# Optimization experiments

Hardware: AMD Instinct MI355X
Metric: run time of the kernel (lower is better)

Reference implementation:

```python
import jax, jax.numpy as jnp
import numpy as np

# ---- constants matching init_kwargs ----
ATOM_DIMS = np.array([119, 5, 12, 12, 10, 6, 6, 2, 2])
OFFSETS = np.concatenate([[0], np.cumsum(ATOM_DIMS)[:-1]])  # per-column offsets into concat table
HID = 256
HEADS = 8
BASES = 4
AGGS = 3  # sum, mean, max
LAYERS = 4
FH = HID // HEADS  # 32
N_GRAPHS = 2048
EPS = 1e-5


def setup_inputs() -> dict:
    key = jax.random.key(0)
    ks = iter(jax.random.split(key, 64))
    N, E = 50000, 800000
    x = jax.random.randint(next(ks), (N, 9), 0, 2, dtype=jnp.int64) if jax.config.jax_enable_x64 else jax.random.randint(next(ks), (N, 9), 0, 2, dtype=jnp.int32)
    edge_index = jax.random.randint(next(ks), (2, E), 0, N, dtype=x.dtype)
    batch = jnp.sort(jax.random.randint(next(ks), (N,), 0, N_GRAPHS, dtype=x.dtype))
    s = 0.05
    atom_emb = jax.random.normal(next(ks), (int(ATOM_DIMS.sum()), HID), jnp.float32) * s
    bases_W = jax.random.normal(next(ks), (LAYERS, HID, BASES * FH), jnp.float32) * s
    comb_W = jax.random.normal(next(ks), (LAYERS, HID, HEADS * BASES * AGGS), jnp.float32) * s
    comb_b = jnp.zeros((LAYERS, HEADS * BASES * AGGS), jnp.float32)
    conv_bias = jnp.zeros((LAYERS, HID), jnp.float32)
    bn_gamma = jnp.ones((LAYERS, HID), jnp.float32)
    bn_beta = jnp.zeros((LAYERS, HID), jnp.float32)
    w1 = jax.random.normal(next(ks), (HID, HID // 2), jnp.float32) * s
    g1 = jnp.ones((HID // 2,), jnp.float32)
    b1 = jnp.zeros((HID // 2,), jnp.float32)
    w2 = jax.random.normal(next(ks), (HID // 2, HID // 4), jnp.float32) * s
    g2 = jnp.ones((HID // 4,), jnp.float32)
    b2 = jnp.zeros((HID // 4,), jnp.float32)
    w3 = jax.random.normal(next(ks), (HID // 4, 1), jnp.float32) * s
    b3 = jnp.zeros((1,), jnp.float32)
    return dict(atom_emb=atom_emb, bases_W=bases_W, comb_W=comb_W, comb_b=comb_b,
                conv_bias=conv_bias, bn_gamma=bn_gamma, bn_beta=bn_beta,
                w1=w1, g1=g1, b1=b1, w2=w2, g2=g2, b2=b2, w3=w3, b3=b3,
                x=x, edge_index=edge_index, batch=batch)


def _bn(h, gamma, beta):
    mu = h.mean(0)
    var = h.var(0)
    return (h - mu) * jax.lax.rsqrt(var + EPS) * gamma + beta


def reference(atom_emb, bases_W, comb_W, comb_b, conv_bias, bn_gamma, bn_beta,
              w1, g1, b1, w2, g2, b2, w3, b3, x, edge_index, batch):
    N = x.shape[0]
    offs = jnp.asarray(OFFSETS, dtype=x.dtype)
    # AtomEncoder: sum of per-column embeddings (concat table + offsets)
    h = atom_emb[x + offs[None, :]].sum(axis=1)  # [N, HID]

    # edges with self-loops (EGConv add_self_loops=True); adj_t transposed: row=dst
    loop = jnp.arange(N, dtype=edge_index.dtype)
    dst = jnp.concatenate([edge_index[0], loop])
    src = jnp.concatenate([edge_index[1], loop])
    deg = jax.ops.segment_sum(jnp.ones_like(dst, jnp.float32), dst, num_segments=N)  # >=1

    for l in range(LAYERS):
        bases = h @ bases_W[l]                      # [N, B*FH]
        wts = (h @ comb_W[l] + comb_b[l]).reshape(N, HEADS, AGGS * BASES)
        msgs = bases[src]                            # [E+N, B*FH]
        agg_sum = jax.ops.segment_sum(msgs, dst, num_segments=N)
        agg_mean = agg_sum / deg[:, None]
        agg_max = jax.ops.segment_max(msgs, dst, num_segments=N)
        agg = jnp.stack([agg_sum, agg_mean, agg_max], axis=1)  # [N, A, B*FH]
        agg = agg.reshape(N, AGGS * BASES, FH)
        out = jnp.einsum('nhk,nkd->nhd', wts, agg).reshape(N, HID) + conv_bias[l]
        out = jax.nn.relu(_bn(out, bn_gamma[l], bn_beta[l]))
        h = h + out

    # global mean pool
    gsum = jax.ops.segment_sum(h, batch, num_segments=N_GRAPHS)
    gcnt = jax.ops.segment_sum(jnp.ones((N,), jnp.float32), batch, num_segments=N_GRAPHS)
    g = gsum / jnp.maximum(gcnt, 1.0)[:, None]

    z = jax.nn.relu(_bn(g @ w1, g1, b1))
    z = jax.nn.relu(_bn(z @ w2, g2, b2))
    return z @ w3 + b3
```

## Files before the change

### kernel.cpp

```cpp
#include <hip/hip_runtime.h>
#include <hip/hip_bf16.h>

#define HID 256
#define NGRAPH 2048

typedef __attribute__((ext_vector_type(8))) short s16x8;
typedef __attribute__((ext_vector_type(4))) float f32x4v;

__device__ inline short f2b(float f) {
    __hip_bfloat16 b = __float2bfloat16(f);
    return *reinterpret_cast<short*>(&b);
}
__device__ inline float b2f_lo(unsigned int v) {
    return __uint_as_float(v << 16);
}
__device__ inline float b2f_hi(unsigned int v) {
    return __uint_as_float(v & 0xffff0000u);
}

__global__ __launch_bounds__(256) void atom_enc(const int* __restrict__ x,
                                                const float* __restrict__ emb,
                                                float* __restrict__ h,
                                                short* __restrict__ hb, int N) {
    int n = blockIdx.x;
    int c = threadIdx.x;
    if (n >= N) return;
    const int offs[9] = {0, 119, 124, 136, 148, 158, 164, 170, 172};
    float s = 0.f;
#pragma unroll
    for (int j = 0; j < 9; ++j) {
        int row = x[n * 9 + j] + offs[j];
        s += emb[row * 256 + c];
    }
    h[n * 256 + c] = s;
    hb[n * 256 + c] = f2b(s);
}

__global__ void prep_wt(const float* __restrict__ bases_W, const float* __restrict__ comb_W,
                        short* __restrict__ WT) {
    int l = blockIdx.x / 224;
    int n = blockIdx.x % 224;
    int k = threadIdx.x;
    float v = (n < 128) ? bases_W[((size_t)l * 256 + k) * 128 + n]
                        : comb_W[((size_t)l * 256 + k) * 96 + (n - 128)];
    WT[((size_t)l * 224 + n) * 256 + k] = f2b(v);
}

__global__ void init_cnt(int* cnt, int N) {
    int i = blockIdx.x * blockDim.x + threadIdx.x;
    if (i < N) cnt[i] = 1;
}

__global__ void csr_count(const int* __restrict__ ei, int E, int* cnt) {
    int e = blockIdx.x * blockDim.x + threadIdx.x;
    if (e >= E) return;
    atomicAdd(&cnt[ei[e]], 1);
}

__global__ __launch_bounds__(256) void scan_s1(const int* __restrict__ cnt, int* __restrict__ blksum, int N) {
    __shared__ int red[256];
    int base = blockIdx.x * 1024;
    int s = 0;
#pragma unroll
    for (int q = 0; q < 4; ++q) {
        int i = base + threadIdx.x * 4 + q;
        s += (i < N) ? cnt[i] : 0;
    }
    red[threadIdx.x] = s;
    __syncthreads();
    for (int off = 128; off > 0; off >>= 1) {
        if (threadIdx.x < off) red[threadIdx.x] += red[threadIdx.x + off];
        __syncthreads();
    }
    if (threadIdx.x == 0) blksum[blockIdx.x] = red[0];
}

__global__ __launch_bounds__(256) void scan_s2(int* __restrict__ blksum, int nb, int* __restrict__ row_ptr, int N) {
    __shared__ int buf[256];
    int v = (threadIdx.x < nb) ? blksum[threadIdx.x] : 0;
    buf[threadIdx.x] = v;
    __syncthreads();
    for (int off = 1; off < 256; off <<= 1) {
        int t = (threadIdx.x >= off) ? buf[threadIdx.x - off] : 0;
        __syncthreads();
        buf[threadIdx.x] += t;
        __syncthreads();
    }
    if (threadIdx.x < nb) blksum[threadIdx.x] = buf[threadIdx.x] - v;
    if (threadIdx.x == 0) row_ptr[N] = buf[255];
}

__global__ __launch_bounds__(256) void scan_s3(const int* __restrict__ cnt, const int* __restrict__ blksum,
                                               int* __restrict__ row_ptr, int* __restrict__ woff, int N) {
    __shared__ int buf[256];
    int base = blockIdx.x * 1024;
    int i0 = base + threadIdx.x * 4;
    int v[4];
    int s = 0;
#pragma unroll
    for (int q = 0; q < 4; ++q) {
        int i = i0 + q;
        v[q] = (i < N) ? cnt[i] : 0;
        s += v[q];
    }
    buf[threadIdx.x] = s;
    __syncthreads();
    for (int off = 1; off < 256; off <<= 1) {
        int t = (threadIdx.x >= off) ? buf[threadIdx.x - off] : 0;
        __syncthreads();
        buf[threadIdx.x] += t;
        __syncthreads();
    }
    int excl = buf[threadIdx.x] - s + blksum[blockIdx.x];
#pragma unroll
    for (int q = 0; q < 4; ++q) {
        int i = i0 + q;
        if (i < N) { row_ptr[i] = excl; woff[i] = excl; }
        excl += v[q];
    }
}

__global__ __launch_bounds__(256) void ph_hist(const int* __restrict__ ei, int E, int T,
                                               int PB, int NBK, int* __restrict__ mcnt) {
    __shared__ int hist[256];
    hist[threadIdx.x] = 0;
    __syncthreads();
    int base = blockIdx.x * 4096;
#pragma unroll
    for (int q = 0; q < 16; ++q) {
        int i = base + q * 256 + threadIdx.x;
        if (i < T) {
            int d = (i < E) ? ei[i] : (i - E);
            atomicAdd(&hist[d >> 8], 1);
        }
    }
    __syncthreads();
    if (threadIdx.x < NBK) mcnt[threadIdx.x * PB + blockIdx.x] = hist[threadIdx.x];
}

__global__ __launch_bounds__(256) void ph_scatter(const int* __restrict__ ei, int E, int T,
                                                  int PB, int NBK, const int* __restrict__ moff,
                                                  uint2* __restrict__ pairs) {
    __shared__ int off[256];
    if (threadIdx.x < NBK) off[threadIdx.x] = moff[threadIdx.x * PB + blockIdx.x];
    __syncthreads();
    int base = blockIdx.x * 4096;
#pragma unroll
    for (int q = 0; q < 16; ++q) {
        int i = base + q * 256 + threadIdx.x;
        if (i < T) {
            int d, s;
            if (i < E) { d = ei[i]; s = ei[E + i]; }
            else       { d = i - E; s = i - E; }
            int pos = atomicAdd(&off[d >> 8], 1);
            pairs[pos] = make_uint2((unsigned)d, (unsigned)s);
        }
    }
}

__global__ __launch_bounds__(256) void ph_sort(const uint2* __restrict__ pairs,
                                               const int* __restrict__ row_ptr,
                                               const int* __restrict__ moff,
                                               int NBK, int PB, int T,
                                               int* __restrict__ srcs) {
    __shared__ int wcnt[256];
    wcnt[threadIdx.x] = 0;
    __syncthreads();
    int bin = blockIdx.x;
    int p0 = moff[bin * PB];
    int p1 = (bin + 1 < NBK) ? moff[(bin + 1) * PB] : T;
    for (int i = p0 + threadIdx.x; i < p1; i += 256) {
        uint2 u = pairs[i];
        int d = (int)u.x;
        int rank = atomicAdd(&wcnt[d & 255], 1);
        srcs[row_ptr[d] + rank] = (int)u.y;
    }
}

__global__ __launch_bounds__(256) void gemm_mfma(const short* __restrict__ hb,
                                                 const short* __restrict__ WT,
                                                 const float* __restrict__ cb,
                                                 short* __restrict__ bases,
                                                 float* __restrict__ wts, int N) {
    __shared__ short bs[2][32 * 256];
    int tid = threadIdx.x;
    int wid = tid >> 6;
    int lane = tid & 63;
    int m0 = blockIdx.x * 64 + wid * 16;
    int row_a = m0 + (lane & 15);
    if (row_a > N - 1) row_a = N - 1;
    int kgrp = (lane >> 4) * 8;

    s16x8 a[8];
#pragma unroll
    for (int i = 0; i < 8; ++i)
        a[i] = *(const s16x8*)&hb[(size_t)row_a * 256 + i * 32 + kgrp];

    int st_col = tid >> 3;
    int st_kk = (tid & 7) * 32;
    int st_sw = (st_col & 7) << 4;
    int st_base = st_col * 512 + st_kk * 2;

    auto stage = [&](int buf, int t) {
        const s16x8* src = (const s16x8*)&WT[(size_t)(t * 32 + st_col) * 256 + st_kk];
        char* dst = (char*)bs[buf];
#pragma unroll
        for (int q = 0; q < 4; ++q)
            *(s16x8*)(dst + ((st_base + q * 16) ^ st_sw)) = src[q];
    };

    stage(0, 0);

    int col = lane & 15;
    int rd_base = col * 512 + (lane >> 4) * 16;
    int rd_sw = (col & 7) << 4;
    int rbase = m0 + (lane >> 4) * 4;

    for (int t = 0; t < 7; ++t) {
        __syncthreads();
        if (t + 1 < 7) stage((t + 1) & 1, t + 1);

        const char* base = (const char*)bs[t & 1];
        f32x4v c0 = {0.f, 0.f, 0.f, 0.f};
        f32x4v c1 = {0.f, 0.f, 0.f, 0.f};
#pragma unroll
        for (int i = 0; i < 8; ++i) {
            s16x8 b0 = *(const s16x8*)(base + ((rd_base + i * 64) ^ rd_sw));
            s16x8 b1 = *(const s16x8*)(base + ((rd_base + 8192 + i * 64) ^ rd_sw));
            c0 = __builtin_amdgcn_mfma_f32_16x16x32_bf16(a[i], b0, c0, 0, 0, 0);
            c1 = __builtin_amdgcn_mfma_f32_16x16x32_bf16(a[i], b1, c1, 0, 0, 0);
        }

        int cc0 = t * 32 + col;
        int cc1 = cc0 + 16;
        float cb0 = (cc0 >= 128) ? cb[cc0 - 128] : 0.f;
        float cb1 = (cc1 >= 128) ? cb[cc1 - 128] : 0.f;
#pragma unroll
        for (int r = 0; r < 4; ++r) {
            int row = rbase + r;
            if (row >= N) continue;
            float v0 = c0[r], v1 = c1[r];
            if (cc0 < 128) bases[(size_t)row * 128 + cc0] = f2b(v0);
            else wts[(size_t)row * 96 + (cc0 - 128)] = v0 + cb0;
            if (cc1 < 128) bases[(size_t)row * 128 + cc1] = f2b(v1);
            else wts[(size_t)row * 96 + (cc1 - 128)] = v1 + cb1;
        }
    }
}

__global__ __launch_bounds__(256) void agg_einsum(const short* __restrict__ bases,
                                                  const float* __restrict__ wts,
                                                  const int* __restrict__ row_ptr,
                                                  const int* __restrict__ srcs,
                                                  const float* __restrict__ cbias,
                                                  float* __restrict__ outp,
                                                  float* __restrict__ partial, int N) {
    __shared__ float agg_lds[4][3][128];
    __shared__ float wts_lds[4][96];
    __shared__ float red[4][256];
    int wid = threadIdx.x >> 6;
    int lane = threadIdx.x & 63;
    int n = blockIdx.x * 4 + wid;
    bool valid = (n < N);

    int r0 = 0, r1 = 0;
    if (valid) {
        r0 = row_ptr[n];
        r1 = row_ptr[n + 1];
        wts_lds[wid][lane] = wts[(size_t)n * 96 + lane];
        if (lane < 32) wts_lds[wid][64 + lane] = wts[(size_t)n * 96 + 64 + lane];
    }

    int g = lane & 31;
    int half = lane >> 5;
    const short* bp = bases + 4 * g;
    const float NI = -3.402823466e+38f;
    float sA0 = 0.f, sA1 = 0.f, sA2 = 0.f, sA3 = 0.f;
    float sB0 = 0.f, sB1 = 0.f, sB2 = 0.f, sB3 = 0.f;
    float mA0 = NI, mA1 = NI, mA2 = NI, mA3 = NI;
    float mB0 = NI, mB1 = NI, mB2 = NI, mB3 = NI;

#define GACC8(S, s0_, s1_, s2_, s3_, m0_, m1_, m2_, m3_)                     \
    {                                                                        \
        uint2 v = *(const uint2*)&bp[(size_t)(S) * 128];                     \
        float f0 = b2f_lo(v.x), f1 = b2f_hi(v.x);                            \
        float f2 = b2f_lo(v.y), f3 = b2f_hi(v.y);                            \
        s0_ += f0; s1_ += f1; s2_ += f2; s3_ += f3;                          \
        m0_ = fmaxf(m0_, f0); m1_ = fmaxf(m1_, f1);                          \
        m2_ = fmaxf(m2_, f2); m3_ = fmaxf(m3_, f3);                          \
    }

    int r = r0;
    while (r < r1) {
        int chunk = r1 - r;
        if (chunk > 64) chunk = 64;
        int sidx = (lane < chunk) ? srcs[r + lane] : 0;
        int npair = chunk >> 1;
        int jp = 0;
        for (; jp + 4 <= npair; jp += 4) {
            int e0 = (jp + 0) * 2 + half, e1 = (jp + 1) * 2 + half;
            int e2 = (jp + 2) * 2 + half, e3 = (jp + 3) * 2 + half;
            int s0 = __shfl(sidx, e0), s1 = __shfl(sidx, e1);
            int s2 = __shfl(sidx, e2), s3 = __shfl(sidx, e3);
            GACC8(s0, sA0, sA1, sA2, sA3, mA0, mA1, mA2, mA3);
            GACC8(s1, sB0, sB1, sB2, sB3, mB0, mB1, mB2, mB3);
            GACC8(s2, sA0, sA1, sA2, sA3, mA0, mA1, mA2, mA3);
            GACC8(s3, sB0, sB1, sB2, sB3, mB0, mB1, mB2, mB3);
        }
        for (; jp < npair; ++jp) {
            int e0 = jp * 2 + half;
            int s0 = __shfl(sidx, e0);
            GACC8(s0, sA0, sA1, sA2, sA3, mA0, mA1, mA2, mA3);
        }
        if (chunk & 1) {
            int s0 = __shfl(sidx, chunk - 1);
            if (half == 0) {
                GACC8(s0, sB0, sB1, sB2, sB3, mB0, mB1, mB2, mB3);
            }
        }
        r += chunk;
    }
#undef GACC8

    float accs[4] = {0.f, 0.f, 0.f, 0.f};
    if (valid) {
        float s0 = sA0 + sB0, s1 = sA1 + sB1, s2 = sA2 + sB2, s3 = sA3 + sB3;
        float m0 = fmaxf(mA0, mB0), m1 = fmaxf(mA1, mB1);
        float m2 = fmaxf(mA2, mB2), m3 = fmaxf(mA3, mB3);
        s0 += __shfl_xor(s0, 32); s1 += __shfl_xor(s1, 32);
        s2 += __shfl_xor(s2, 32); s3 += __shfl_xor(s3, 32);
        m0 = fmaxf(m0, __shfl_xor(m0, 32)); m1 = fmaxf(m1, __shfl_xor(m1, 32));
        m2 = fmaxf(m2, __shfl_xor(m2, 32)); m3 = fmaxf(m3, __shfl_xor(m3, 32));

        float inv = 1.0f / (float)(r1 - r0);
        if (half == 0) {
            float4 sv = make_float4(s0, s1, s2, s3);
            float4 mv = make_float4(s0 * inv, s1 * inv, s2 * inv, s3 * inv);
            float4 xv = make_float4(m0, m1, m2, m3);
            *(float4*)&agg_lds[wid][0][4 * g] = sv;
            *(float4*)&agg_lds[wid][1][4 * g] = mv;
            *(float4*)&agg_lds[wid][2][4 * g] = xv;
        }

        asm volatile("s_waitcnt lgkmcnt(0)" ::: "memory");

#pragma unroll
        for (int j = 0; j < 4; ++j) {
            int o = lane + 64 * j;
            int hh = o >> 5;
            int d = o & 31;
            float acc = cbias[o];
#pragma unroll
            for (int k = 0; k < 12; ++k)
                acc = fmaf(wts_lds[wid][hh * 12 + k], agg_lds[wid][k >> 2][(k & 3) * 32 + d], acc);
            outp[n * 256 + o] = acc;
            accs[j] = acc;
        }
    }
#pragma unroll
    for (int j = 0; j < 4; ++j) red[wid][lane + 64 * j] = accs[j];
    __syncthreads();
    int c = threadIdx.x;
    float s = (red[0][c] + red[1][c]) + (red[2][c] + red[3][c]);
    float s2 = (red[0][c] * red[0][c] + red[1][c] * red[1][c]) +
               (red[2][c] * red[2][c] + red[3][c] * red[3][c]);
    partial[((size_t)blockIdx.x * 2 + 0) * 256 + c] = s;
    partial[((size_t)blockIdx.x * 2 + 1) * 256 + c] = s2;
}

__global__ __launch_bounds__(256) void bn_reduce(const float* __restrict__ partial, int NB,
                                                 float* __restrict__ partial2) {
    int t = threadIdx.x;
    int chunk = (NB + 255) / 256;
    int rbeg = blockIdx.x * chunk;
    int rend = min(NB, rbeg + chunk);
    float s = 0.f, s2 = 0.f;
    for (int r = rbeg; r < rend; ++r) {
        s += partial[((size_t)r * 2 + 0) * 256 + t];
        s2 += partial[((size_t)r * 2 + 1) * 256 + t];
    }
    partial2[((size_t)blockIdx.x * 2 + 0) * 256 + t] = s;
    partial2[((size_t)blockIdx.x * 2 + 1) * 256 + t] = s2;
}

__global__ void bn_stats(const float* __restrict__ v, int N, int C, float* __restrict__ partial) {
    int c = threadIdx.x;
    float s = 0.f, s2 = 0.f;
    for (int r = blockIdx.x; r < N; r += gridDim.x) {
        float t = v[r * C + c];
        s += t; s2 += t * t;
    }
    partial[(blockIdx.x * 2 + 0) * C + c] = s;
    partial[(blockIdx.x * 2 + 1) * C + c] = s2;
}

__global__ __launch_bounds__(256) void bn_finalize(const float* __restrict__ partial, int NB, int C, int N,
                                                   const float* __restrict__ gamma, const float* __restrict__ beta,
                                                   float* __restrict__ ss) {
    int c = blockIdx.x;
    float s = 0.f, s2 = 0.f;
    for (int b = threadIdx.x; b < NB; b += 256) {
        s += partial[((size_t)b * 2 + 0) * C + c];
        s2 += partial[((size_t)b * 2 + 1) * C + c];
    }
#pragma unroll
    for (int off = 32; off > 0; off >>= 1) {
        s += __shfl_down(s, off);
        s2 += __shfl_down(s2, off);
    }
    __shared__ float wsum[4][2];
    int wid = threadIdx.x >> 6;
    int lane = threadIdx.x & 63;
    if (lane == 0) { wsum[wid][0] = s; wsum[wid][1] = s2; }
    __syncthreads();
    if (threadIdx.x == 0) {
        s = (wsum[0][0] + wsum[1][0]) + (wsum[2][0] + wsum[3][0]);
        s2 = (wsum[0][1] + wsum[1][1]) + (wsum[2][1] + wsum[3][1]);
        float invN = 1.0f / (float)N;
        float mu = s * invN;
        float var = fmaxf(s2 * invN - mu * mu, 0.f);
        float sc = gamma[c] * rsqrtf(var + 1e-5f);
        ss[c] = sc;
        ss[C + c] = beta[c] - mu * sc;
    }
}

__global__ void bn_apply_res4(float4* __restrict__ h, const float4* __restrict__ outp,
                              const float* __restrict__ ss, short* __restrict__ hb,
                              int total4, int write_hb) {
    int i = blockIdx.x * blockDim.x + threadIdx.x;
    if (i >= total4) return;
    int c0 = (i * 4) & 255;
    float4 o = outp[i];
    float4 hv = h[i];
    hv.x += fmaxf(o.x * ss[c0 + 0] + ss[256 + c0 + 0], 0.f);
    hv.y += fmaxf(o.y * ss[c0 + 1] + ss[256 + c0 + 1], 0.f);
    hv.z += fmaxf(o.z * ss[c0 + 2] + ss[256 + c0 + 2], 0.f);
    hv.w += fmaxf(o.w * ss[c0 + 3] + ss[256 + c0 + 3], 0.f);
    h[i] = hv;
    if (write_hb) {
        short4 hb4;
        hb4.x = f2b(hv.x); hb4.y = f2b(hv.y); hb4.z = f2b(hv.z); hb4.w = f2b(hv.w);
        *(short4*)&hb[(size_t)i * 4] = hb4;
    }
}

__global__ void bn_apply(float* __restrict__ z, const float* __restrict__ ss, int total, int C, int Cmask) {
    int i = blockIdx.x * blockDim.x + threadIdx.x;
    if (i >= total) return;
    int c = i & Cmask;
    z[i] = fmaxf(z[i] * ss[c] + ss[C + c], 0.f);
}

__device__ int lower_bound_dev(const int* a, int n, int v) {
    int lo = 0, hi = n;
    while (lo < hi) {
        int mid = (lo + hi) >> 1;
        if (a[mid] < v) lo = mid + 1; else hi = mid;
    }
    return lo;
}

__global__ __launch_bounds__(256) void pool_kernel(const float* __restrict__ h,
                                                   const int* __restrict__ batch, int N,
                                                   float* __restrict__ g) {
    __shared__ int sh[2];
    if (threadIdx.x == 0) {
        sh[0] = lower_bound_dev(batch, N, (int)blockIdx.x);
        sh[1] = lower_bound_dev(batch, N, (int)blockIdx.x + 1);
    }
    __syncthreads();
    int s0 = sh[0], s1 = sh[1];
    float s = 0.f;
    for (int r = s0; r < s1; ++r) s += h[r * 256 + threadIdx.x];
    float cnt = (float)(s1 - s0);
    g[blockIdx.x * 256 + threadIdx.x] = s / fmaxf(cnt, 1.0f);
}

__global__ void mlp_gemm(const float* __restrict__ in, const float* __restrict__ W,
                         float* __restrict__ outp, int K, int C) {
    extern __shared__ float srow[];
    int r = blockIdx.x;
    for (int k = threadIdx.x; k < K; k += blockDim.x) srow[k] = in[r * K + k];
    __syncthreads();
    int c = threadIdx.x;
    float acc = 0.f;
    for (int k = 0; k < K; ++k) acc = fmaf(srow[k], W[k * C + c], acc);
    outp[r * C + c] = acc;
}

__global__ void final_gemm(const float* __restrict__ z2, const float* __restrict__ w3,
                           const float* __restrict__ b3, float* __restrict__ outp, int G) {
    int g = blockIdx.x * blockDim.x + threadIdx.x;
    if (g >= G) return;
    float acc = b3[0];
    for (int k = 0; k < 64; ++k) acc = fmaf(z2[g * 64 + k], w3[k], acc);
    outp[g] = acc;
}

extern "C" void kernel_launch(void* const* d_in, const int* in_sizes, int n_in,
                              void* d_out, int out_size, void* d_ws, size_t ws_size,
                              hipStream_t stream) {
    const float* atom_emb = (const float*)d_in[0];
    const float* bases_W = (const float*)d_in[1];
    const float* comb_W = (const float*)d_in[2];
    const float* comb_b = (const float*)d_in[3];
    const float* conv_bias = (const float*)d_in[4];
    const float* bn_gamma = (const float*)d_in[5];
    const float* bn_beta = (const float*)d_in[6];
    const float* w1 = (const float*)d_in[7];
    const float* g1 = (const float*)d_in[8];
    const float* b1 = (const float*)d_in[9];
    const float* w2 = (const float*)d_in[10];
    const float* g2 = (const float*)d_in[11];
    const float* b2 = (const float*)d_in[12];
    const float* w3 = (const float*)d_in[13];
    const float* b3 = (const float*)d_in[14];
    const int* x = (const int*)d_in[15];
    const int* edge_index = (const int*)d_in[16];
    const int* batch = (const int*)d_in[17];
    float* out = (float*)d_out;

    const int N = in_sizes[15] / 9;
    const int E = in_sizes[16] / 2;
    const int G = NGRAPH;
    const int T = E + N;
    const int NCHUNK = (N + 1023) / 1024;
    const int PB = (T + 4095) / 4096;
    const int NBK = (N + 255) >> 8;
    const int M = NBK * PB;
    const int MCHUNK = (M + 1023) / 1024;
    const int AGG_NB = (N + 3) / 4;

    char* p = (char*)d_ws;
    auto alloc = [&](size_t bytes) -> void* {
        void* r = (void*)p;
        p += (bytes + 255) & ~(size_t)255;
        return r;
    };
    float* h = (float*)alloc((size_t)N * 256 * 4);
    short* hb = (short*)alloc((size_t)N * 256 * 2);
    float* outb = (float*)alloc((size_t)N * 256 * 4);
    short* bases = (short*)alloc((size_t)N * 128 * 2);
    float* wts = (float*)alloc((size_t)N * 96 * 4);
    short* WT = (short*)alloc((size_t)4 * 224 * 256 * 2);
    int* row_ptr = (int*)alloc((size_t)(N + 1) * 4);
    int* cnt = (int*)alloc((size_t)N * 4);
    int* woff = (int*)alloc((size_t)N * 4);
    int* blksum = (int*)alloc((size_t)256 * 4);
    int* mcnt = (int*)alloc((size_t)(M + 1) * 4);
    int* moff = (int*)alloc((size_t)(M + 1) * 4);
    int* srcs = (int*)alloc((size_t)T * 4);
    float* partial = (float*)alloc((size_t)AGG_NB * 2 * 256 * 4);
    float* partial2 = (float*)alloc((size_t)256 * 2 * 256 * 4);
    float* ss = (float*)alloc((size_t)2 * 256 * 4);
    float* g = (float*)alloc((size_t)G * 256 * 4);
    float* z1 = (float*)alloc((size_t)G * 128 * 4);
    float* z2 = (float*)alloc((size_t)G * 64 * 4);
    uint2* pairs = (uint2*)outb;

    atom_enc<<<N, 256, 0, stream>>>(x, atom_emb, h, hb, N);
    prep_wt<<<4 * 224, 256, 0, stream>>>(bases_W, comb_W, WT);

    init_cnt<<<(N + 255) / 256, 256, 0, stream>>>(cnt, N);
    csr_count<<<(E + 255) / 256, 256, 0, stream>>>(edge_index, E, cnt);
    scan_s1<<<NCHUNK, 256, 0, stream>>>(cnt, blksum, N);
    scan_s2<<<1, 256, 0, stream>>>(blksum, NCHUNK, row_ptr, N);
    scan_s3<<<NCHUNK, 256, 0, stream>>>(cnt, blksum, row_ptr, woff, N);

    ph_hist<<<PB, 256, 0, stream>>>(edge_index, E, T, PB, NBK, mcnt);
    scan_s1<<<MCHUNK, 256, 0, stream>>>(mcnt, blksum, M);
    scan_s2<<<1, 256, 0, stream>>>(blksum, MCHUNK, moff, M);
    scan_s3<<<MCHUNK, 256, 0, stream>>>(mcnt, blksum, moff, moff, M);
    ph_scatter<<<PB, 256, 0, stream>>>(edge_index, E, T, PB, NBK, moff, pairs);
    ph_sort<<<NBK, 256, 0, stream>>>(pairs, row_ptr, moff, NBK, PB, T, srcs);

    for (int l = 0; l < 4; ++l) {
        const short* WTl = WT + (size_t)l * 224 * 256;
        const float* cb = comb_b + (size_t)l * 96;
        const float* cbias = conv_bias + (size_t)l * 256;
        const float* gam = bn_gamma + (size_t)l * 256;
        const float* bet = bn_beta + (size_t)l * 256;

        gemm_mfma<<<(N + 63) / 64, 256, 0, stream>>>(hb, WTl, cb, bases, wts, N);
        agg_einsum<<<AGG_NB, 256, 0, stream>>>(bases, wts, row_ptr, srcs, cbias, outb, partial, N);
        bn_reduce<<<256, 256, 0, stream>>>(partial, AGG_NB, partial2);
        bn_finalize<<<256, 256, 0, stream>>>(partial2, 256, 256, N, gam, bet, ss);
        int total4 = N * 256 / 4;
        bn_apply_res4<<<(total4 + 255) / 256, 256, 0, stream>>>((float4*)h, (const float4*)outb, ss, hb,
                                                                total4, l < 3 ? 1 : 0);
    }

    pool_kernel<<<G, 256, 0, stream>>>(h, batch, N, g);

    mlp_gemm<<<G, 128, 256 * 4, stream>>>(g, w1, z1, 256, 128);
    bn_stats<<<64, 128, 0, stream>>>(z1, G, 128, partial);
    bn_finalize<<<128, 256, 0, stream>>>(partial, 64, 128, G, g1, b1, ss);
    bn_apply<<<(G * 128 + 255) / 256, 256, 0, stream>>>(z1, ss, G * 128, 128, 127);

    mlp_gemm<<<G, 64, 128 * 4, stream>>>(z1, w2, z2, 128, 64);
    bn_stats<<<64, 64, 0, stream>>>(z2, G, 64, partial);
    bn_finalize<<<64, 256, 0, stream>>>(partial, 64, 64, G, g2, b2, ss);
    bn_apply<<<(G * 64 + 255) / 256, 256, 0, stream>>>(z2, ss, G * 64, 64, 63);

    final_gemm<<<(G + 255) / 256, 256, 0, stream>>>(z2, w3, b3, out, G);
}
```

Measured before the change: 635.2 us.

## Fuse BN-apply residual into next layer GEMM prologue and process two nodes per wave

```diff
diff --git a/kernel.cpp b/kernel.cpp
--- a/kernel.cpp
+++ b/kernel.cpp
@@ -20,8 +20,7 @@
 
 __global__ __launch_bounds__(256) void atom_enc(const int* __restrict__ x,
                                                 const float* __restrict__ emb,
-                                                float* __restrict__ h,
-                                                short* __restrict__ hb, int N) {
+                                                float* __restrict__ h, int N) {
     int n = blockIdx.x;
     int c = threadIdx.x;
     if (n >= N) return;
@@ -33,7 +32,6 @@
         s += emb[row * 256 + c];
     }
     h[n * 256 + c] = s;
-    hb[n * 256 + c] = f2b(s);
 }
 
 __global__ void prep_wt(const float* __restrict__ bases_W, const float* __restrict__ comb_W,
@@ -177,24 +175,68 @@
     }
 }
 
-__global__ __launch_bounds__(256) void gemm_mfma(const short* __restrict__ hb,
+__global__ __launch_bounds__(256) void gemm_mfma(const float* h,
+                                                 const float* __restrict__ outb,
+                                                 const float* __restrict__ ss,
+                                                 int do_bn,
                                                  const short* __restrict__ WT,
                                                  const float* __restrict__ cb,
                                                  short* __restrict__ bases,
-                                                 float* __restrict__ wts, int N) {
+                                                 float* __restrict__ wts,
+                                                 float* hw, int N) {
     __shared__ short bs[2][32 * 256];
     int tid = threadIdx.x;
     int wid = tid >> 6;
     int lane = tid & 63;
     int m0 = blockIdx.x * 64 + wid * 16;
-    int row_a = m0 + (lane & 15);
-    if (row_a > N - 1) row_a = N - 1;
+    int row_orig = m0 + (lane & 15);
+    bool owner = (row_orig < N);
+    int row_a = owner ? row_orig : (N - 1);
     int kgrp = (lane >> 4) * 8;
 
     s16x8 a[8];
-#pragma unroll
-    for (int i = 0; i < 8; ++i)
-        a[i] = *(const s16x8*)&hb[(size_t)row_a * 256 + i * 32 + kgrp];
+    if (do_bn) {
+#pragma unroll
+        for (int i = 0; i < 8; ++i) {
+            int cbase = i * 32 + kgrp;
+            size_t base = (size_t)row_a * 256 + cbase;
+            float4 h0 = *(const float4*)&h[base];
+            float4 h1 = *(const float4*)&h[base + 4];
+            float4 o0 = *(const float4*)&outb[base];
+            float4 o1 = *(const float4*)&outb[base + 4];
+            float4 sc0 = *(const float4*)&ss[cbase];
+            float4 sc1 = *(const float4*)&ss[cbase + 4];
+            float4 sh0 = *(const float4*)&ss[256 + cbase];
+            float4 sh1 = *(const float4*)&ss[256 + cbase + 4];
+            h0.x += fmaxf(o0.x * sc0.x + sh0.x, 0.f);
+            h0.y += fmaxf(o0.y * sc0.y + sh0.y, 0.f);
+            h0.z += fmaxf(o0.z * sc0.z + sh0.z, 0.f);
+            h0.w += fmaxf(o0.w * sc0.w + sh0.w, 0.f);
+            h1.x += fmaxf(o1.x * sc1.x + sh1.x, 0.f);
+            h1.y += fmaxf(o1.y * sc1.y + sh1.y, 0.f);
+            h1.z += fmaxf(o1.z * sc1.z + sh1.z, 0.f);
+            h1.w += fmaxf(o1.w * sc1.w + sh1.w, 0.f);
+            if (owner) {
+                *(float4*)&hw[base] = h0;
+                *(float4*)&hw[base + 4] = h1;
+            }
+            s16x8 t;
+            t[0] = f2b(h0.x); t[1] = f2b(h0.y); t[2] = f2b(h0.z); t[3] = f2b(h0.w);
+            t[4] = f2b(h1.x); t[5] = f2b(h1.y); t[6] = f2b(h1.z); t[7] = f2b(h1.w);
+            a[i] = t;
+        }
+    } else {
+#pragma unroll
+        for (int i = 0; i < 8; ++i) {
+            size_t base = (size_t)row_a * 256 + i * 32 + kgrp;
+            float4 h0 = *(const float4*)&h[base];
+            float4 h1 = *(const float4*)&h[base + 4];
+            s16x8 t;
+            t[0] = f2b(h0.x); t[1] = f2b(h0.y); t[2] = f2b(h0.z); t[3] = f2b(h0.w);
+            t[4] = f2b(h1.x); t[5] = f2b(h1.y); t[6] = f2b(h1.z); t[7] = f2b(h1.w);
+            a[i] = t;
+        }
+    }
 
     int st_col = tid >> 3;
     int st_kk = (tid & 7) * 32;
@@ -257,28 +299,33 @@
                                                   float* __restrict__ partial, int N) {
     __shared__ float agg_lds[4][3][128];
     __shared__ float wts_lds[4][96];
-    __shared__ float red[4][256];
+    __shared__ float redS[4][256];
+    __shared__ float redQ[4][256];
     int wid = threadIdx.x >> 6;
     int lane = threadIdx.x & 63;
-    int n = blockIdx.x * 4 + wid;
-    bool valid = (n < N);
-
-    int r0 = 0, r1 = 0;
-    if (valid) {
-        r0 = row_ptr[n];
-        r1 = row_ptr[n + 1];
-        wts_lds[wid][lane] = wts[(size_t)n * 96 + lane];
-        if (lane < 32) wts_lds[wid][64 + lane] = wts[(size_t)n * 96 + 64 + lane];
-    }
-
     int g = lane & 31;
     int half = lane >> 5;
     const short* bp = bases + 4 * g;
     const float NI = -3.402823466e+38f;
-    float sA0 = 0.f, sA1 = 0.f, sA2 = 0.f, sA3 = 0.f;
-    float sB0 = 0.f, sB1 = 0.f, sB2 = 0.f, sB3 = 0.f;
-    float mA0 = NI, mA1 = NI, mA2 = NI, mA3 = NI;
-    float mB0 = NI, mB1 = NI, mB2 = NI, mB3 = NI;
+
+    float pS[4] = {0.f, 0.f, 0.f, 0.f};
+    float pQ[4] = {0.f, 0.f, 0.f, 0.f};
+
+    for (int nn = 0; nn < 2; ++nn) {
+        int n = blockIdx.x * 8 + wid * 2 + nn;
+        bool valid = (n < N);
+        int r0 = 0, r1 = 0;
+        if (valid) {
+            r0 = row_ptr[n];
+            r1 = row_ptr[n + 1];
+            wts_lds[wid][lane] = wts[(size_t)n * 96 + lane];
+            if (lane < 32) wts_lds[wid][64 + lane] = wts[(size_t)n * 96 + 64 + lane];
+        }
+
+        float sA0 = 0.f, sA1 = 0.f, sA2 = 0.f, sA3 = 0.f;
+        float sB0 = 0.f, sB1 = 0.f, sB2 = 0.f, sB3 = 0.f;
+        float mA0 = NI, mA1 = NI, mA2 = NI, mA3 = NI;
+        float mB0 = NI, mB1 = NI, mB2 = NI, mB3 = NI;
 
 #define GACC8(S, s0_, s1_, s2_, s3_, m0_, m1_, m2_, m3_)                     \
     {                                                                        \
@@ -290,80 +337,84 @@
         m2_ = fmaxf(m2_, f2); m3_ = fmaxf(m3_, f3);                          \
     }
 
-    int r = r0;
-    while (r < r1) {
-        int chunk = r1 - r;
-        if (chunk > 64) chunk = 64;
-        int sidx = (lane < chunk) ? srcs[r + lane] : 0;
-        int npair = chunk >> 1;
-        int jp = 0;
-        for (; jp + 4 <= npair; jp += 4) {
-            int e0 = (jp + 0) * 2 + half, e1 = (jp + 1) * 2 + half;
-            int e2 = (jp + 2) * 2 + half, e3 = (jp + 3) * 2 + half;
-            int s0 = __shfl(sidx, e0), s1 = __shfl(sidx, e1);
-            int s2 = __shfl(sidx, e2), s3 = __shfl(sidx, e3);
-            GACC8(s0, sA0, sA1, sA2, sA3, mA0, mA1, mA2, mA3);
-            GACC8(s1, sB0, sB1, sB2, sB3, mB0, mB1, mB2, mB3);
-            GACC8(s2, sA0, sA1, sA2, sA3, mA0, mA1, mA2, mA3);
-            GACC8(s3, sB0, sB1, sB2, sB3, mB0, mB1, mB2, mB3);
-        }
-        for (; jp < npair; ++jp) {
-            int e0 = jp * 2 + half;
-            int s0 = __shfl(sidx, e0);
-            GACC8(s0, sA0, sA1, sA2, sA3, mA0, mA1, mA2, mA3);
-        }
-        if (chunk & 1) {
-            int s0 = __shfl(sidx, chunk - 1);
+        int r = r0;
+        while (r < r1) {
+            int chunk = r1 - r;
+            if (chunk > 64) chunk = 64;
+            int sidx = (lane < chunk) ? srcs[r + lane] : 0;
+            int npair = chunk >> 1;
+            int jp = 0;
+            for (; jp + 4 <= npair; jp += 4) {
+                int e0 = (jp + 0) * 2 + half, e1 = (jp + 1) * 2 + half;
+                int e2 = (jp + 2) * 2 + half, e3 = (jp + 3) * 2 + half;
+                int s0 = __shfl(sidx, e0), s1 = __shfl(sidx, e1);
+                int s2 = __shfl(sidx, e2), s3 = __shfl(sidx, e3);
+                GACC8(s0, sA0, sA1, sA2, sA3, mA0, mA1, mA2, mA3);
+                GACC8(s1, sB0, sB1, sB2, sB3, mB0, mB1, mB2, mB3);
+                GACC8(s2, sA0, sA1, sA2, sA3, mA0, mA1, mA2, mA3);
+                GACC8(s3, sB0, sB1, sB2, sB3, mB0, mB1, mB2, mB3);
+            }
+            for (; jp < npair; ++jp) {
+                int e0 = jp * 2 + half;
+                int s0 = __shfl(sidx, e0);
+                GACC8(s0, sA0, sA1, sA2, sA3, mA0, mA1, mA2, mA3);
+            }
+            if (chunk & 1) {
+                int s0 = __shfl(sidx, chunk - 1);
+                if (half == 0) {
+                    GACC8(s0, sB0, sB1, sB2, sB3, mB0, mB1, mB2, mB3);
+                }
+            }
+            r += chunk;
+        }
+#undef GACC8
+
+        if (valid) {
+            float s0 = sA0 + sB0, s1 = sA1 + sB1, s2 = sA2 + sB2, s3 = sA3 + sB3;
+            float m0 = fmaxf(mA0, mB0), m1 = fmaxf(mA1, mB1);
+            float m2 = fmaxf(mA2, mB2), m3 = fmaxf(mA3, mB3);
+            s0 += __shfl_xor(s0, 32); s1 += __shfl_xor(s1, 32);
+            s2 += __shfl_xor(s2, 32); s3 += __shfl_xor(s3, 32);
+            m0 = fmaxf(m0, __shfl_xor(m0, 32)); m1 = fmaxf(m1, __shfl_xor(m1, 32));
+            m2 = fmaxf(m2, __shfl_xor(m2, 32)); m3 = fmaxf(m3, __shfl_xor(m3, 32));
+
+            float inv = 1.0f / (float)(r1 - r0);
             if (half == 0) {
-                GACC8(s0, sB0, sB1, sB2, sB3, mB0, mB1, mB2, mB3);
+                float4 sv = make_float4(s0, s1, s2, s3);
+                float4 mv = make_float4(s0 * inv, s1 * inv, s2 * inv, s3 * inv);
+                float4 xv = make_float4(m0, m1, m2, m3);
+                *(float4*)&agg_lds[wid][0][4 * g] = sv;
+                *(float4*)&agg_lds[wid][1][4 * g] = mv;
+                *(float4*)&agg_lds[wid][2][4 * g] = xv;
             }
-        }
-        r += chunk;
-    }
-#undef GACC8
-
-    float accs[4] = {0.f, 0.f, 0.f, 0.f};
-    if (valid) {
-        float s0 = sA0 + sB0, s1 = sA1 + sB1, s2 = sA2 + sB2, s3 = sA3 + sB3;
-        float m0 = fmaxf(mA0, mB0), m1 = fmaxf(mA1, mB1);
-        float m2 = fmaxf(mA2, mB2), m3 = fmaxf(mA3, mB3);
-        s0 += __shfl_xor(s0, 32); s1 += __shfl_xor(s1, 32);
-        s2 += __shfl_xor(s2, 32); s3 += __shfl_xor(s3, 32);
-        m0 = fmaxf(m0, __shfl_xor(m0, 32)); m1 = fmaxf(m1, __shfl_xor(m1, 32));
-        m2 = fmaxf(m2, __shfl_xor(m2, 32)); m3 = fmaxf(m3, __shfl_xor(m3, 32));
-
-        float inv = 1.0f / (float)(r1 - r0);
-        if (half == 0) {
-            float4 sv = make_float4(s0, s1, s2, s3);
-            float4 mv = make_float4(s0 * inv, s1 * inv, s2 * inv, s3 * inv);
-            float4 xv = make_float4(m0, m1, m2, m3);
-            *(float4*)&agg_lds[wid][0][4 * g] = sv;
-            *(float4*)&agg_lds[wid][1][4 * g] = mv;
-            *(float4*)&agg_lds[wid][2][4 * g] = xv;
-        }
-
-        asm volatile("s_waitcnt lgkmcnt(0)" ::: "memory");
-
-#pragma unroll
-        for (int j = 0; j < 4; ++j) {
-            int o = lane + 64 * j;
-            int hh = o >> 5;
-            int d = o & 31;
-            float acc = cbias[o];
-#pragma unroll
-            for (int k = 0; k < 12; ++k)
-                acc = fmaf(wts_lds[wid][hh * 12 + k], agg_lds[wid][k >> 2][(k & 3) * 32 + d], acc);
-            outp[n * 256 + o] = acc;
-            accs[j] = acc;
-        }
-    }
-#pragma unroll
-    for (int j = 0; j < 4; ++j) red[wid][lane + 64 * j] = accs[j];
+
+            asm volatile("s_waitcnt lgkmcnt(0)" ::: "memory");
+
+#pragma unroll
+            for (int j = 0; j < 4; ++j) {
+                int o = lane + 64 * j;
+                int hh = o >> 5;
+                int d = o & 31;
+                float acc = cbias[o];
+#pragma unroll
+                for (int k = 0; k < 12; ++k)
+                    acc = fmaf(wts_lds[wid][hh * 12 + k], agg_lds[wid][k >> 2][(k & 3) * 32 + d], acc);
+                outp[n * 256 + o] = acc;
+                pS[j] += acc;
+                pQ[j] += acc * acc;
+            }
+        }
+    }
+
+#pragma unroll
+    for (int j = 0; j < 4; ++j) {
+        redS[wid][lane + 64 * j] = pS[j];
+        redQ[wid][lane + 64 * j] = pQ[j];
+    }
     __syncthreads();
     int c = threadIdx.x;
-    float s = (red[0][c] + red[1][c]) + (red[2][c] + red[3][c]);
-    float s2 = (red[0][c] * red[0][c] + red[1][c] * red[1][c]) +
-               (red[2][c] * red[2][c] + red[3][c] * red[3][c]);
+    float s = (redS[0][c] + redS[1][c]) + (redS[2][c] + redS[3][c]);
+    float s2 = (redQ[0][c] + redQ[1][c]) + (redQ[2][c] + redQ[3][c]);
     partial[((size_t)blockIdx.x * 2 + 0) * 256 + c] = s;
     partial[((size_t)blockIdx.x * 2 + 1) * 256 + c] = s2;
 }
@@ -426,8 +477,7 @@
 }
 
 __global__ void bn_apply_res4(float4* __restrict__ h, const float4* __restrict__ outp,
-                              const float* __restrict__ ss, short* __restrict__ hb,
-                              int total4, int write_hb) {
+                              const float* __restrict__ ss, int total4) {
     int i = blockIdx.x * blockDim.x + threadIdx.x;
     if (i >= total4) return;
     int c0 = (i * 4) & 255;
@@ -438,11 +488,6 @@
     hv.z += fmaxf(o.z * ss[c0 + 2] + ss[256 + c0 + 2], 0.f);
     hv.w += fmaxf(o.w * ss[c0 + 3] + ss[256 + c0 + 3], 0.f);
     h[i] = hv;
-    if (write_hb) {
-        short4 hb4;
-        hb4.x = f2b(hv.x); hb4.y = f2b(hv.y); hb4.z = f2b(hv.z); hb4.w = f2b(hv.w);
-        *(short4*)&hb[(size_t)i * 4] = hb4;
-    }
 }
 
 __global__ void bn_apply(float* __restrict__ z, const float* __restrict__ ss, int total, int C, int Cmask) {
@@ -530,7 +575,7 @@
     const int NBK = (N + 255) >> 8;
     const int M = NBK * PB;
     const int MCHUNK = (M + 1023) / 1024;
-    const int AGG_NB = (N + 3) / 4;
+    const int AGG_NB = (N + 7) / 8;
 
     char* p = (char*)d_ws;
     auto alloc = [&](size_t bytes) -> void* {
@@ -539,7 +584,6 @@
         return r;
     };
     float* h = (float*)alloc((size_t)N * 256 * 4);
-    short* hb = (short*)alloc((size_t)N * 256 * 2);
     float* outb = (float*)alloc((size_t)N * 256 * 4);
     short* bases = (short*)alloc((size_t)N * 128 * 2);
     float* wts = (float*)alloc((size_t)N * 96 * 4);
@@ -559,7 +603,7 @@
     float* z2 = (float*)alloc((size_t)G * 64 * 4);
     uint2* pairs = (uint2*)outb;
 
-    atom_enc<<<N, 256, 0, stream>>>(x, atom_emb, h, hb, N);
+    atom_enc<<<N, 256, 0, stream>>>(x, atom_emb, h, N);
     prep_wt<<<4 * 224, 256, 0, stream>>>(bases_W, comb_W, WT);
 
     init_cnt<<<(N + 255) / 256, 256, 0, stream>>>(cnt, N);
@@ -582,13 +626,15 @@
         const float* gam = bn_gamma + (size_t)l * 256;
         const float* bet = bn_beta + (size_t)l * 256;
 
-        gemm_mfma<<<(N + 63) / 64, 256, 0, stream>>>(hb, WTl, cb, bases, wts, N);
+        gemm_mfma<<<(N + 63) / 64, 256, 0, stream>>>(h, outb, ss, l > 0 ? 1 : 0,
+                                                     WTl, cb, bases, wts, h, N);
         agg_einsum<<<AGG_NB, 256, 0, stream>>>(bases, wts, row_ptr, srcs, cbias, outb, partial, N);
         bn_reduce<<<256, 256, 0, stream>>>(partial, AGG_NB, partial2);
         bn_finalize<<<256, 256, 0, stream>>>(partial2, 256, 256, N, gam, bet, ss);
+    }
+    {
         int total4 = N * 256 / 4;
-        bn_apply_res4<<<(total4 + 255) / 256, 256, 0, stream>>>((float4*)h, (const float4*)outb, ss, hb,
-                                                                total4, l < 3 ? 1 : 0);
+        bn_apply_res4<<<(total4 + 255) / 256, 256, 0, stream>>>((float4*)h, (const float4*)outb, ss, total4);
     }
 
     pool_kernel<<<G, 256, 0, stream>>>(h, batch, N, g);
```

After: 632.5 us. Within noise of the previous version (-0.4%).

## Fuse BN-apply residual into next layer's GEMM load and store activations in bf16

Applied to the files above, without the earlier changes.

```diff
diff --git a/kernel.cpp b/kernel.cpp
--- a/kernel.cpp
+++ b/kernel.cpp
@@ -11,6 +11,9 @@
     __hip_bfloat16 b = __float2bfloat16(f);
     return *reinterpret_cast<short*>(&b);
 }
+__device__ inline float b2f(short s) {
+    return __uint_as_float(((unsigned)(unsigned short)s) << 16);
+}
 __device__ inline float b2f_lo(unsigned int v) {
     return __uint_as_float(v << 16);
 }
@@ -20,7 +23,6 @@
 
 __global__ __launch_bounds__(256) void atom_enc(const int* __restrict__ x,
                                                 const float* __restrict__ emb,
-                                                float* __restrict__ h,
                                                 short* __restrict__ hb, int N) {
     int n = blockIdx.x;
     int c = threadIdx.x;
@@ -32,7 +34,6 @@
         int row = x[n * 9 + j] + offs[j];
         s += emb[row * 256 + c];
     }
-    h[n * 256 + c] = s;
     hb[n * 256 + c] = f2b(s);
 }
 
@@ -177,7 +178,10 @@
     }
 }
 
-__global__ __launch_bounds__(256) void gemm_mfma(const short* __restrict__ hb,
+__global__ __launch_bounds__(256) void gemm_mfma(short* hb,
+                                                 const short* __restrict__ outb,
+                                                 const float* __restrict__ ss,
+                                                 int do_bn,
                                                  const short* __restrict__ WT,
                                                  const float* __restrict__ cb,
                                                  short* __restrict__ bases,
@@ -187,14 +191,39 @@
     int wid = tid >> 6;
     int lane = tid & 63;
     int m0 = blockIdx.x * 64 + wid * 16;
-    int row_a = m0 + (lane & 15);
-    if (row_a > N - 1) row_a = N - 1;
+    int row_orig = m0 + (lane & 15);
+    bool owner = (row_orig < N);
+    int row_a = owner ? row_orig : (N - 1);
     int kgrp = (lane >> 4) * 8;
 
     s16x8 a[8];
-#pragma unroll
-    for (int i = 0; i < 8; ++i)
-        a[i] = *(const s16x8*)&hb[(size_t)row_a * 256 + i * 32 + kgrp];
+    if (do_bn) {
+#pragma unroll
+        for (int i = 0; i < 8; ++i) {
+            int cbase = i * 32 + kgrp;
+            size_t base = (size_t)row_a * 256 + cbase;
+            s16x8 hv = *(const s16x8*)&hb[base];
+            s16x8 ov = *(const s16x8*)&outb[base];
+            s16x8 t;
+#pragma unroll
+            for (int k = 0; k < 8; ++k) {
+                float hf = b2f(hv[k]);
+                float of = b2f(ov[k]);
+                float sc = ss[cbase + k];
+                float sh = ss[256 + cbase + k];
+                hf += fmaxf(of * sc + sh, 0.f);
+                t[k] = f2b(hf);
+            }
+            if (owner) *(s16x8*)&hb[base] = t;
+            a[i] = t;
+        }
+    } else {
+#pragma unroll
+        for (int i = 0; i < 8; ++i) {
+            size_t base = (size_t)row_a * 256 + i * 32 + kgrp;
+            a[i] = *(const s16x8*)&hb[base];
+        }
+    }
 
     int st_col = tid >> 3;
     int st_kk = (tid & 7) * 32;
@@ -253,7 +282,7 @@
                                                   const int* __restrict__ row_ptr,
                                                   const int* __restrict__ srcs,
                                                   const float* __restrict__ cbias,
-                                                  float* __restrict__ outp,
+                                                  short* __restrict__ outp,
                                                   float* __restrict__ partial, int N) {
     __shared__ float agg_lds[4][3][128];
     __shared__ float wts_lds[4][96];
@@ -353,7 +382,7 @@
 #pragma unroll
             for (int k = 0; k < 12; ++k)
                 acc = fmaf(wts_lds[wid][hh * 12 + k], agg_lds[wid][k >> 2][(k & 3) * 32 + d], acc);
-            outp[n * 256 + o] = acc;
+            outp[(size_t)n * 256 + o] = f2b(acc);
             accs[j] = acc;
         }
     }
@@ -425,24 +454,23 @@
     }
 }
 
-__global__ void bn_apply_res4(float4* __restrict__ h, const float4* __restrict__ outp,
-                              const float* __restrict__ ss, short* __restrict__ hb,
-                              int total4, int write_hb) {
+__global__ void bn_apply_res8(short* __restrict__ hb, const short* __restrict__ outp,
+                              const float* __restrict__ ss, int total8) {
     int i = blockIdx.x * blockDim.x + threadIdx.x;
-    if (i >= total4) return;
-    int c0 = (i * 4) & 255;
-    float4 o = outp[i];
-    float4 hv = h[i];
-    hv.x += fmaxf(o.x * ss[c0 + 0] + ss[256 + c0 + 0], 0.f);
-    hv.y += fmaxf(o.y * ss[c0 + 1] + ss[256 + c0 + 1], 0.f);
-    hv.z += fmaxf(o.z * ss[c0 + 2] + ss[256 + c0 + 2], 0.f);
-    hv.w += fmaxf(o.w * ss[c0 + 3] + ss[256 + c0 + 3], 0.f);
-    h[i] = hv;
-    if (write_hb) {
-        short4 hb4;
-        hb4.x = f2b(hv.x); hb4.y = f2b(hv.y); hb4.z = f2b(hv.z); hb4.w = f2b(hv.w);
-        *(short4*)&hb[(size_t)i * 4] = hb4;
-    }
+    if (i >= total8) return;
+    int c0 = (i * 8) & 255;
+    size_t base = (size_t)i * 8;
+    s16x8 hv = *(const s16x8*)&hb[base];
+    s16x8 ov = *(const s16x8*)&outp[base];
+    s16x8 t;
+#pragma unroll
+    for (int k = 0; k < 8; ++k) {
+        float hf = b2f(hv[k]);
+        float of = b2f(ov[k]);
+        hf += fmaxf(of * ss[c0 + k] + ss[256 + c0 + k], 0.f);
+        t[k] = f2b(hf);
+    }
+    *(s16x8*)&hb[base] = t;
 }
 
 __global__ void bn_apply(float* __restrict__ z, const float* __restrict__ ss, int total, int C, int Cmask) {
@@ -461,7 +489,7 @@
     return lo;
 }
 
-__global__ __launch_bounds__(256) void pool_kernel(const float* __restrict__ h,
+__global__ __launch_bounds__(256) void pool_kernel(const short* __restrict__ hb,
                                                    const int* __restrict__ batch, int N,
                                                    float* __restrict__ g) {
     __shared__ int sh[2];
@@ -472,7 +500,7 @@
     __syncthreads();
     int s0 = sh[0], s1 = sh[1];
     float s = 0.f;
-    for (int r = s0; r < s1; ++r) s += h[r * 256 + threadIdx.x];
+    for (int r = s0; r < s1; ++r) s += b2f(hb[(size_t)r * 256 + threadIdx.x]);
     float cnt = (float)(s1 - s0);
     g[blockIdx.x * 256 + threadIdx.x] = s / fmaxf(cnt, 1.0f);
 }
@@ -538,9 +566,8 @@
         p += (bytes + 255) & ~(size_t)255;
         return r;
     };
-    float* h = (float*)alloc((size_t)N * 256 * 4);
     short* hb = (short*)alloc((size_t)N * 256 * 2);
-    float* outb = (float*)alloc((size_t)N * 256 * 4);
+    short* outb = (short*)alloc((size_t)N * 256 * 2);
     short* bases = (short*)alloc((size_t)N * 128 * 2);
     float* wts = (float*)alloc((size_t)N * 96 * 4);
     short* WT = (short*)alloc((size_t)4 * 224 * 256 * 2);
@@ -557,9 +584,9 @@
     float* g = (float*)alloc((size_t)G * 256 * 4);
     float* z1 = (float*)alloc((size_t)G * 128 * 4);
     float* z2 = (float*)alloc((size_t)G * 64 * 4);
-    uint2* pairs = (uint2*)outb;
-
-    atom_enc<<<N, 256, 0, stream>>>(x, atom_emb, h, hb, N);
+    uint2* pairs = (uint2*)alloc((size_t)T * 8);
+
+    atom_enc<<<N, 256, 0, stream>>>(x, atom_emb, hb, N);
     prep_wt<<<4 * 224, 256, 0, stream>>>(bases_W, comb_W, WT);
 
     init_cnt<<<(N + 255) / 256, 256, 0, stream>>>(cnt, N);
@@ -582,16 +609,18 @@
         const float* gam = bn_gamma + (size_t)l * 256;
         const float* bet = bn_beta + (size_t)l * 256;
 
-        gemm_mfma<<<(N + 63) / 64, 256, 0, stream>>>(hb, WTl, cb, bases, wts, N);
+        gemm_mfma<<<(N + 63) / 64, 256, 0, stream>>>(hb, outb, ss, l > 0 ? 1 : 0,
+                                                     WTl, cb, bases, wts, N);
         agg_einsum<<<AGG_NB, 256, 0, stream>>>(bases, wts, row_ptr, srcs, cbias, outb, partial, N);
         bn_reduce<<<256, 256, 0, stream>>>(partial, AGG_NB, partial2);
         bn_finalize<<<256, 256, 0, stream>>>(partial2, 256, 256, N, gam, bet, ss);
-        int total4 = N * 256 / 4;
-        bn_apply_res4<<<(total4 + 255) / 256, 256, 0, stream>>>((float4*)h, (const float4*)outb, ss, hb,
-                                                                total4, l < 3 ? 1 : 0);
-    }
-
-    pool_kernel<<<G, 256, 0, stream>>>(h, batch, N, g);
+    }
+    {
+        int total8 = N * 256 / 8;
+        bn_apply_res8<<<(total8 + 255) / 256, 256, 0, stream>>>(hb, outb, ss, total8);
+    }
+
+    pool_kernel<<<G, 256, 0, stream>>>(hb, batch, N, g);
 
     mlp_gemm<<<G, 128, 256 * 4, stream>>>(g, w1, z1, 256, 128);
     bn_stats<<<64, 128, 0, stream>>>(z1, G, 128, partial);
```

Result: faster. 567.7 us (-10.6%).
